# Kernel tuning notes

Measured on AMD Instinct MI355X. Metric: run time of the kernel, lower is better.

Reference implementation:

```python
import jax, jax.numpy as jnp
import numpy as np

B = 16384        # batch
P = 8            # num policies (experts)
D = 512          # latent dim
A = 64           # action dim
H = 1024         # hidden dim


def setup_inputs() -> dict:
    key = jax.random.key(0)
    ks = jax.random.split(key, 7)
    latents = jax.random.normal(ks[0], (B, D), dtype=jnp.float32)
    actions = jax.random.normal(ks[1], (B, A), dtype=jnp.float32)
    policy_indices = jax.random.randint(ks[2], (B,), 0, P, dtype=jnp.int64)
    # Per-policy 2-layer MLP params: concat(latent, action) -> hidden -> latent
    scale1 = 1.0 / np.sqrt(D + A)
    scale2 = 1.0 / np.sqrt(H)
    W1 = jax.random.normal(ks[3], (P, D + A, H), dtype=jnp.float32) * scale1
    b1 = jnp.zeros((P, H), dtype=jnp.float32)
    W2 = jax.random.normal(ks[4], (P, H, D), dtype=jnp.float32) * scale2
    b2 = jnp.zeros((P, D), dtype=jnp.float32)
    return {"latents": latents, "actions": actions, "policy_indices": policy_indices,
            "W1": W1, "b1": b1, "W2": W2, "b2": b2}


def reference(latents, actions, policy_indices, W1, b1, W2, b2):
    # Original: for each policy i, route rows with policy_indices == i through
    # that policy's dynamics model; scatter results back into next_latents.
    # Equivalent dense form: run all experts, then select per-row expert output.
    x = jnp.concatenate([latents, actions], axis=-1)          # [B, D+A]
    h = jax.nn.relu(jnp.einsum('bd,pdh->bph', x, W1) + b1)    # [B, P, H]
    y = jnp.einsum('bph,phd->bpd', h, W2) + b2                # [B, P, D]
    idx = policy_indices[:, None, None]                       # [B, 1, 1]
    next_latents = jnp.take_along_axis(y, idx, axis=1)[:, 0]  # [B, D]
    return next_latents
```

## Files before the change

### kernel.cpp

```cpp
#include <hip/hip_runtime.h>
#include <hip/hip_bf16.h>
#include <stdint.h>

#define B_SZ 16384
#define P_SZ 8
#define D_SZ 512
#define A_SZ 64
#define K1 576
#define H_SZ 1024
#define NSEG 64
#define MB_MAX 72
#define BPAD (B_SZ + P_SZ*256)
#define PREP_BLOCKS (BPAD * 72 / 256)
#define TR1_BLOCKS (P_SZ * 9 * 16)
#define TR2_BLOCKS (P_SZ * 16 * 8)
#define G1_GRID (BPAD / 128 * (H_SZ / 128))
#define G2_GRID (BPAD / 128 * (D_SZ / 64))

typedef __bf16 bf16_t;
typedef __bf16 bf16x8 __attribute__((ext_vector_type(8)));
typedef float f32x4 __attribute__((ext_vector_type(4)));

__device__ __forceinline__ void glds16(const void* g, void* l) {
    __builtin_amdgcn_global_load_lds(
        (const __attribute__((address_space(1))) unsigned*)g,
        (__attribute__((address_space(3))) unsigned*)l, 16, 0, 0);
}


__global__ __launch_bounds__(256) void hist_block(const int* __restrict__ pol,
                                                  int* __restrict__ blockhist,
                                                  int* __restrict__ rowidx) {
    __shared__ int lc[P_SZ];
    int t = threadIdx.x;
    if (t < P_SZ) lc[t] = 0;
    __syncthreads();
    int gid = blockIdx.x * 256 + t;
    rowidx[gid] = -1;
    if (gid < BPAD - B_SZ) rowidx[B_SZ + gid] = -1;
    atomicAdd(&lc[pol[gid]], 1);
    __syncthreads();
    if (t < P_SZ) blockhist[blockIdx.x * P_SZ + t] = lc[t];
}

__global__ __launch_bounds__(256) void prefix_kernel(const int* __restrict__ blockhist,
                                                     int* __restrict__ counts,
                                                     int* __restrict__ cursors,
                                                     int* __restrict__ blk_p) {
    __shared__ int csh[P_SZ];
    int t = threadIdx.x;
    int p = t >> 5, i = t & 31;
    int s = blockhist[i * P_SZ + p] + blockhist[(i + 32) * P_SZ + p];
#pragma unroll
    for (int m = 16; m >= 1; m >>= 1) s += __shfl_xor(s, m, 32);
    if (i == 0) csh[p] = s;
    __syncthreads();
    if (t == 0) {
        int run = 0;
        for (int pp = 0; pp < P_SZ; ++pp) {
            counts[pp] = csh[pp];
            cursors[pp] = run;
            run += ((csh[pp] + 255) >> 8) * 256;
        }
    }
    if (t < MB_MAX) {
        int run = 0, val = -1;
#pragma unroll
        for (int pp = 0; pp < P_SZ; ++pp) {
            int nb = (csh[pp] + 255) >> 8;
            if (t >= run && t < run + nb) val = pp;
            run += nb;
        }
        blk_p[t] = val;
    }
}

__global__ __launch_bounds__(256) void scatter_agg(const int* __restrict__ pol,
                                                   int* __restrict__ cursors,
                                                   int* __restrict__ rowidx) {
    __shared__ int lc[P_SZ], base_s[P_SZ];
    int t = threadIdx.x;
    if (t < P_SZ) lc[t] = 0;
    __syncthreads();
    int i = blockIdx.x * 256 + t;
    int p = pol[i];
    int lpos = atomicAdd(&lc[p], 1);
    __syncthreads();
    if (t < P_SZ) base_s[t] = atomicAdd(&cursors[t], lc[t]);
    __syncthreads();
    rowidx[base_s[p] + lpos] = i;
}


__global__ __launch_bounds__(256) void prep_all(const float* __restrict__ latents,
                                                const float* __restrict__ actions,
                                                const int* __restrict__ rowidx,
                                                const float* __restrict__ W1,
                                                const float* __restrict__ W2,
                                                bf16_t* __restrict__ xs,
                                                bf16_t* __restrict__ w1t,
                                                bf16_t* __restrict__ w2t) {
    int bx = blockIdx.x;
    int tid = threadIdx.x;
    if (bx < PREP_BLOCKS) {
        int idx = bx * 256 + tid;
        int s = idx / 72;
        int col = (idx - s * 72) * 8;
        int g = rowidx[s];
        bf16x8 o;
        if (g < 0) {
            o = (bf16x8){0,0,0,0,0,0,0,0};
        } else {
            const float* src;
            if (col < D_SZ) src = latents + (size_t)g * D_SZ + col;
            else            src = actions + (size_t)g * A_SZ + (col - D_SZ);
            f32x4 v0 = *(const f32x4*)src;
            f32x4 v1 = *(const f32x4*)(src + 4);
            o[0] = (bf16_t)v0[0]; o[1] = (bf16_t)v0[1]; o[2] = (bf16_t)v0[2]; o[3] = (bf16_t)v0[3];
            o[4] = (bf16_t)v1[0]; o[5] = (bf16_t)v1[1]; o[6] = (bf16_t)v1[2]; o[7] = (bf16_t)v1[3];
        }
        *(bf16x8*)(xs + (size_t)s * K1 + col) = o;
        return;
    }
    int tz = bx - PREP_BLOCKS;
    const float* Wp; bf16_t* WTp; int K, N, k0, n0;
    if (tz < TR1_BLOCKS) {
        int p = tz / 144, rem = tz % 144;
        k0 = (rem / 16) * 64; n0 = (rem % 16) * 64;
        K = K1; N = H_SZ;
        Wp = W1 + (size_t)p * K1 * H_SZ;
        WTp = w1t + (size_t)p * H_SZ * K1;
    } else {
        int u = tz - TR1_BLOCKS;
        int p = u / 128, rem = u % 128;
        k0 = (rem / 8) * 64; n0 = (rem % 8) * 64;
        K = H_SZ; N = D_SZ;
        Wp = W2 + (size_t)p * H_SZ * D_SZ;
        WTp = w2t + (size_t)p * D_SZ * H_SZ;
    }
    __shared__ float ls[64][65];
#pragma unroll
    for (int e = 0; e < 4; ++e) {
        int idx = e * 256 + tid;
        int kk = idx >> 4, nn = (idx & 15) * 4;
        f32x4 v = *(const f32x4*)&Wp[(size_t)(k0 + kk) * N + n0 + nn];
        ls[kk][nn]     = v[0];
        ls[kk][nn + 1] = v[1];
        ls[kk][nn + 2] = v[2];
        ls[kk][nn + 3] = v[3];
    }
    __syncthreads();
#pragma unroll
    for (int e = 0; e < 2; ++e) {
        int idx = e * 256 + tid;
        int nn = idx >> 3, ks = (idx & 7) * 8;
        bf16x8 o;
#pragma unroll
        for (int q = 0; q < 8; ++q) o[q] = (bf16_t)ls[ks + q][nn];
        *(bf16x8*)&WTp[(size_t)(n0 + nn) * K + k0 + ks] = o;
    }
}


__global__ __launch_bounds__(256, 3) void gemm1_kernel(
    const bf16_t* __restrict__ xs, const bf16_t* __restrict__ w1t,
    const float* __restrict__ b1, const int* __restrict__ blk_p,
    bf16_t* __restrict__ h) {

    const int b = blockIdx.x;
    const int wid = (b & 7) * (G1_GRID / 8) + (b >> 3);
    const int mb = wid >> 3;
    const int nb = wid & 7;
    const int p = blk_p[mb >> 1];
    if (p < 0) return;
    const int m0 = mb * 128;
    const int n0 = nb * 128;

    constexpr int SUB = 128 * 32;
    __shared__ __align__(16) bf16_t As[2 * SUB];
    __shared__ __align__(16) bf16_t Bs[2 * SUB];

    const int tid = threadIdx.x;
    const int wave = tid >> 6, lane = tid & 63;

    const bf16_t *a_src[2][2], *b_src[2][2];
    bf16_t *a_dst[2][2], *b_dst[2][2];
#pragma unroll
    for (int hh = 0; hh < 2; ++hh)
#pragma unroll
        for (int i = 0; i < 2; ++i) {
            int c = (wave * 2 + i) * 64 + lane;
            int r = c >> 2;
            int kl = (c & 3) ^ ((r >> 1) & 3);
            a_src[hh][i] = xs + (size_t)(m0 + r) * K1 + hh * 32 + kl * 8;
            a_dst[hh][i] = As + hh * SUB + c * 8;
            b_src[hh][i] = w1t + ((size_t)p * H_SZ + n0 + r) * K1 + hh * 32 + kl * 8;
            b_dst[hh][i] = Bs + hh * SUB + c * 8;
        }

    const int l16 = lane & 15, qd = lane >> 4;
    const int swz = (l16 >> 1) & 3;
    const int wr = wave >> 1, wc = wave & 1;
    int aoff[4], boff[4];
#pragma unroll
    for (int i = 0; i < 4; ++i) aoff[i] = (wr * 64 + i * 16 + l16) * 32 + ((qd ^ swz) * 8);
#pragma unroll
    for (int j = 0; j < 4; ++j) boff[j] = (wc * 64 + j * 16 + l16) * 32 + ((qd ^ swz) * 8);

    f32x4 acc[4][4];
#pragma unroll
    for (int i = 0; i < 4; ++i)
#pragma unroll
        for (int j = 0; j < 4; ++j)
            acc[i][j] = (f32x4){0.f, 0.f, 0.f, 0.f};

    for (int kt = 0; kt < K1; kt += 64) {
        __syncthreads();
#pragma unroll
        for (int hh = 0; hh < 2; ++hh)
#pragma unroll
            for (int i = 0; i < 2; ++i) {
                glds16(a_src[hh][i] + kt, a_dst[hh][i]);
                glds16(b_src[hh][i] + kt, b_dst[hh][i]);
            }
        __syncthreads();
#pragma unroll
        for (int hh = 0; hh < 2; ++hh) {
            bf16x8 af[4], bfv[4];
#pragma unroll
            for (int i = 0; i < 4; ++i) af[i] = *(const bf16x8*)(As + hh * SUB + aoff[i]);
#pragma unroll
            for (int j = 0; j < 4; ++j) bfv[j] = *(const bf16x8*)(Bs + hh * SUB + boff[j]);
#pragma unroll
            for (int i = 0; i < 4; ++i)
#pragma unroll
                for (int j = 0; j < 4; ++j)
                    acc[i][j] = __builtin_amdgcn_mfma_f32_16x16x32_bf16(af[i], bfv[j], acc[i][j], 0, 0, 0);
        }
    }

#pragma unroll
    for (int i = 0; i < 4; ++i) {
#pragma unroll
        for (int r = 0; r < 4; ++r) {
            int ml = wr * 64 + i * 16 + qd * 4 + r;
            size_t row = (size_t)(m0 + ml);
#pragma unroll
            for (int j = 0; j < 4; ++j) {
                int n = n0 + wc * 64 + j * 16 + l16;
                float v = acc[i][j][r] + b1[p * H_SZ + n];
                h[row * H_SZ + n] = (bf16_t)fmaxf(v, 0.f);
            }
        }
    }
}

__global__ __launch_bounds__(256, 4) void gemm2_kernel(
    const bf16_t* __restrict__ h, const bf16_t* __restrict__ w2t,
    const float* __restrict__ b2, const int* __restrict__ blk_p,
    const int* __restrict__ rowidx, float* __restrict__ out) {

    const int b = blockIdx.x;
    const int wid = (b & 7) * (G2_GRID / 8) + (b >> 3);
    const int mb = wid >> 3;
    const int nb = wid & 7;
    const int p = blk_p[mb >> 1];
    if (p < 0) return;
    const int m0 = mb * 128;
    const int n0 = nb * 64;

    constexpr int ASUB = 128 * 32;
    constexpr int BSUB = 64 * 32;
    __shared__ __align__(16) bf16_t As[2 * ASUB];
    __shared__ __align__(16) bf16_t Bs[2 * BSUB];

    const int tid = threadIdx.x;
    const int wave = tid >> 6, lane = tid & 63;

    const bf16_t *a_src[2][2]; bf16_t *a_dst[2][2];
#pragma unroll
    for (int hh = 0; hh < 2; ++hh)
#pragma unroll
        for (int i = 0; i < 2; ++i) {
            int c = (wave * 2 + i) * 64 + lane;
            int r = c >> 2;
            int kl = (c & 3) ^ ((r >> 1) & 3);
            a_src[hh][i] = h + (size_t)(m0 + r) * H_SZ + hh * 32 + kl * 8;
            a_dst[hh][i] = As + hh * ASUB + c * 8;
        }
    const bf16_t *b_src[2]; bf16_t *b_dst[2];
#pragma unroll
    for (int hh = 0; hh < 2; ++hh) {
        int c = wave * 64 + lane;
        int r = c >> 2;
        int kl = (c & 3) ^ ((r >> 1) & 3);
        b_src[hh] = w2t + ((size_t)p * D_SZ + n0 + r) * H_SZ + hh * 32 + kl * 8;
        b_dst[hh] = Bs + hh * BSUB + c * 8;
    }

    const int l16 = lane & 15, qd = lane >> 4;
    const int swz = (l16 >> 1) & 3;
    const int wr = wave >> 1, wc = wave & 1;
    int aoff[4], boff[2];
#pragma unroll
    for (int i = 0; i < 4; ++i) aoff[i] = (wr * 64 + i * 16 + l16) * 32 + ((qd ^ swz) * 8);
#pragma unroll
    for (int j = 0; j < 2; ++j) boff[j] = (wc * 32 + j * 16 + l16) * 32 + ((qd ^ swz) * 8);

    f32x4 acc[4][2];
#pragma unroll
    for (int i = 0; i < 4; ++i)
#pragma unroll
        for (int j = 0; j < 2; ++j)
            acc[i][j] = (f32x4){0.f, 0.f, 0.f, 0.f};

    for (int kt = 0; kt < H_SZ; kt += 64) {
        __syncthreads();
#pragma unroll
        for (int hh = 0; hh < 2; ++hh) {
#pragma unroll
            for (int i = 0; i < 2; ++i) glds16(a_src[hh][i] + kt, a_dst[hh][i]);
            glds16(b_src[hh] + kt, b_dst[hh]);
        }
        __syncthreads();
#pragma unroll
        for (int hh = 0; hh < 2; ++hh) {
            bf16x8 af[4], bfv[2];
#pragma unroll
            for (int i = 0; i < 4; ++i) af[i] = *(const bf16x8*)(As + hh * ASUB + aoff[i]);
#pragma unroll
            for (int j = 0; j < 2; ++j) bfv[j] = *(const bf16x8*)(Bs + hh * BSUB + boff[j]);
#pragma unroll
            for (int i = 0; i < 4; ++i)
#pragma unroll
                for (int j = 0; j < 2; ++j)
                    acc[i][j] = __builtin_amdgcn_mfma_f32_16x16x32_bf16(af[i], bfv[j], acc[i][j], 0, 0, 0);
        }
    }

#pragma unroll
    for (int i = 0; i < 4; ++i) {
#pragma unroll
        for (int r = 0; r < 4; ++r) {
            int ml = wr * 64 + i * 16 + qd * 4 + r;
            int g = rowidx[m0 + ml];
            if (g >= 0) {
                size_t orow = (size_t)g * D_SZ;
#pragma unroll
                for (int j = 0; j < 2; ++j) {
                    int n = n0 + wc * 32 + j * 16 + l16;
                    out[orow + n] = acc[i][j][r] + b2[p * D_SZ + n];
                }
            }
        }
    }
}


extern "C" void kernel_launch(void* const* d_in, const int* in_sizes, int n_in,
                              void* d_out, int out_size, void* d_ws, size_t ws_size,
                              hipStream_t stream) {
    const float* latents = (const float*)d_in[0];
    const float* actions = (const float*)d_in[1];
    const int*   pol     = (const int*)d_in[2];
    const float* W1      = (const float*)d_in[3];
    const float* b1      = (const float*)d_in[4];
    const float* W2      = (const float*)d_in[5];
    const float* b2      = (const float*)d_in[6];
    float* out = (float*)d_out;

    char* ws = (char*)d_ws;
    int* counts    = (int*)ws;
    int* cursors   = counts + P_SZ;
    int* blk_p     = cursors + P_SZ;
    int* blockhist = blk_p + MB_MAX;
    int* rowidx    = blockhist + NSEG * P_SZ;
    size_t pos = ((size_t)(2 * P_SZ + MB_MAX + NSEG * P_SZ + BPAD) * sizeof(int) + 255) & ~(size_t)255;
    bf16_t* xs  = (bf16_t*)(ws + pos);  pos += (size_t)BPAD * K1 * 2;
    bf16_t* hbuf= (bf16_t*)(ws + pos);  pos += (size_t)BPAD * H_SZ * 2;
    bf16_t* w1t = (bf16_t*)(ws + pos);  pos += (size_t)P_SZ * H_SZ * K1 * 2;
    bf16_t* w2t = (bf16_t*)(ws + pos);  pos += (size_t)P_SZ * D_SZ * H_SZ * 2;

    hist_block<<<NSEG, 256, 0, stream>>>(pol, blockhist, rowidx);
    prefix_kernel<<<1, 256, 0, stream>>>(blockhist, counts, cursors, blk_p);
    scatter_agg<<<NSEG, 256, 0, stream>>>(pol, cursors, rowidx);
    prep_all<<<PREP_BLOCKS + TR1_BLOCKS + TR2_BLOCKS, 256, 0, stream>>>(
        latents, actions, rowidx, W1, W2, xs, w1t, w2t);
    gemm1_kernel<<<G1_GRID, 256, 0, stream>>>(xs, w1t, b1, blk_p, hbuf);
    gemm2_kernel<<<G2_GRID, 256, 0, stream>>>(hbuf, w2t, b2, blk_p, rowidx, out);
}
```

Before: 192.6 us.

## Double-buffer LDS tiles in both GEMMs to overlap global loads with MFMA

Both grouped GEMM kernels now hold two LDS buffers per operand. Each iteration issues the async global-to-LDS loads for the next K-tile right after a single barrier, then runs MFMAs on the current tile, so memory latency overlaps with compute and one of the two barriers per iteration is gone. This doubles LDS use per block, so the launch-bounds occupancy hints drop from 3 to 2 (gemm1) and from 4 to 3 (gemm2). Fewer resident blocks per CU can hide less latency across warps.

```diff
diff --git a/kernel.cpp b/kernel.cpp
--- a/kernel.cpp
+++ b/kernel.cpp
@@ -162,7 +162,7 @@
 }
 
 
-__global__ __launch_bounds__(256, 3) void gemm1_kernel(
+__global__ __launch_bounds__(256, 2) void gemm1_kernel(
     const bf16_t* __restrict__ xs, const bf16_t* __restrict__ w1t,
     const float* __restrict__ b1, const int* __restrict__ blk_p,
     bf16_t* __restrict__ h) {
@@ -177,14 +177,15 @@
     const int n0 = nb * 128;
 
     constexpr int SUB = 128 * 32;
-    __shared__ __align__(16) bf16_t As[2 * SUB];
-    __shared__ __align__(16) bf16_t Bs[2 * SUB];
+    constexpr int BUF = 2 * SUB;
+    __shared__ __align__(16) bf16_t As[2 * BUF];
+    __shared__ __align__(16) bf16_t Bs[2 * BUF];
 
     const int tid = threadIdx.x;
     const int wave = tid >> 6, lane = tid & 63;
 
     const bf16_t *a_src[2][2], *b_src[2][2];
-    bf16_t *a_dst[2][2], *b_dst[2][2];
+    int a_slot[2][2], b_slot[2][2];
 #pragma unroll
     for (int hh = 0; hh < 2; ++hh)
 #pragma unroll
@@ -193,10 +194,23 @@
             int r = c >> 2;
             int kl = (c & 3) ^ ((r >> 1) & 3);
             a_src[hh][i] = xs + (size_t)(m0 + r) * K1 + hh * 32 + kl * 8;
-            a_dst[hh][i] = As + hh * SUB + c * 8;
             b_src[hh][i] = w1t + ((size_t)p * H_SZ + n0 + r) * K1 + hh * 32 + kl * 8;
-            b_dst[hh][i] = Bs + hh * SUB + c * 8;
-        }
+            a_slot[hh][i] = hh * SUB + c * 8;
+            b_slot[hh][i] = hh * SUB + c * 8;
+        }
+
+    auto stage = [&](int kt, int buf) {
+        const int bo = buf * BUF;
+#pragma unroll
+        for (int hh = 0; hh < 2; ++hh)
+#pragma unroll
+            for (int i = 0; i < 2; ++i) {
+                glds16(a_src[hh][i] + kt, As + bo + a_slot[hh][i]);
+                glds16(b_src[hh][i] + kt, Bs + bo + b_slot[hh][i]);
+            }
+    };
+
+    stage(0, 0);
 
     const int l16 = lane & 15, qd = lane >> 4;
     const int swz = (l16 >> 1) & 3;
@@ -214,23 +228,18 @@
         for (int j = 0; j < 4; ++j)
             acc[i][j] = (f32x4){0.f, 0.f, 0.f, 0.f};
 
-    for (int kt = 0; kt < K1; kt += 64) {
+    constexpr int NT = K1 / 64;
+    for (int t = 0; t < NT; ++t) {
         __syncthreads();
-#pragma unroll
-        for (int hh = 0; hh < 2; ++hh)
-#pragma unroll
-            for (int i = 0; i < 2; ++i) {
-                glds16(a_src[hh][i] + kt, a_dst[hh][i]);
-                glds16(b_src[hh][i] + kt, b_dst[hh][i]);
-            }
-        __syncthreads();
+        if (t + 1 < NT) stage((t + 1) * 64, (t + 1) & 1);
+        const int bo = (t & 1) * BUF;
 #pragma unroll
         for (int hh = 0; hh < 2; ++hh) {
             bf16x8 af[4], bfv[4];
 #pragma unroll
-            for (int i = 0; i < 4; ++i) af[i] = *(const bf16x8*)(As + hh * SUB + aoff[i]);
-#pragma unroll
-            for (int j = 0; j < 4; ++j) bfv[j] = *(const bf16x8*)(Bs + hh * SUB + boff[j]);
+            for (int i = 0; i < 4; ++i) af[i] = *(const bf16x8*)(As + bo + hh * SUB + aoff[i]);
+#pragma unroll
+            for (int j = 0; j < 4; ++j) bfv[j] = *(const bf16x8*)(Bs + bo + hh * SUB + boff[j]);
 #pragma unroll
             for (int i = 0; i < 4; ++i)
 #pragma unroll
@@ -255,7 +264,7 @@
     }
 }
 
-__global__ __launch_bounds__(256, 4) void gemm2_kernel(
+__global__ __launch_bounds__(256, 3) void gemm2_kernel(
     const bf16_t* __restrict__ h, const bf16_t* __restrict__ w2t,
     const float* __restrict__ b2, const int* __restrict__ blk_p,
     const int* __restrict__ rowidx, float* __restrict__ out) {
@@ -270,14 +279,16 @@
     const int n0 = nb * 64;
 
     constexpr int ASUB = 128 * 32;
+    constexpr int ABUF = 2 * ASUB;
     constexpr int BSUB = 64 * 32;
-    __shared__ __align__(16) bf16_t As[2 * ASUB];
-    __shared__ __align__(16) bf16_t Bs[2 * BSUB];
+    constexpr int BBUF = 2 * BSUB;
+    __shared__ __align__(16) bf16_t As[2 * ABUF];
+    __shared__ __align__(16) bf16_t Bs[2 * BBUF];
 
     const int tid = threadIdx.x;
     const int wave = tid >> 6, lane = tid & 63;
 
-    const bf16_t *a_src[2][2]; bf16_t *a_dst[2][2];
+    const bf16_t *a_src[2][2]; int a_slot[2][2];
 #pragma unroll
     for (int hh = 0; hh < 2; ++hh)
 #pragma unroll
@@ -286,17 +297,29 @@
             int r = c >> 2;
             int kl = (c & 3) ^ ((r >> 1) & 3);
             a_src[hh][i] = h + (size_t)(m0 + r) * H_SZ + hh * 32 + kl * 8;
-            a_dst[hh][i] = As + hh * ASUB + c * 8;
-        }
-    const bf16_t *b_src[2]; bf16_t *b_dst[2];
+            a_slot[hh][i] = hh * ASUB + c * 8;
+        }
+    const bf16_t *b_src[2]; int b_slot[2];
 #pragma unroll
     for (int hh = 0; hh < 2; ++hh) {
         int c = wave * 64 + lane;
         int r = c >> 2;
         int kl = (c & 3) ^ ((r >> 1) & 3);
         b_src[hh] = w2t + ((size_t)p * D_SZ + n0 + r) * H_SZ + hh * 32 + kl * 8;
-        b_dst[hh] = Bs + hh * BSUB + c * 8;
-    }
+        b_slot[hh] = hh * BSUB + c * 8;
+    }
+
+    auto stage = [&](int kt, int buf) {
+#pragma unroll
+        for (int hh = 0; hh < 2; ++hh) {
+#pragma unroll
+            for (int i = 0; i < 2; ++i)
+                glds16(a_src[hh][i] + kt, As + buf * ABUF + a_slot[hh][i]);
+            glds16(b_src[hh] + kt, Bs + buf * BBUF + b_slot[hh]);
+        }
+    };
+
+    stage(0, 0);
 
     const int l16 = lane & 15, qd = lane >> 4;
     const int swz = (l16 >> 1) & 3;
@@ -314,22 +337,19 @@
         for (int j = 0; j < 2; ++j)
             acc[i][j] = (f32x4){0.f, 0.f, 0.f, 0.f};
 
-    for (int kt = 0; kt < H_SZ; kt += 64) {
+    constexpr int NT = H_SZ / 64;
+    for (int t = 0; t < NT; ++t) {
         __syncthreads();
-#pragma unroll
-        for (int hh = 0; hh < 2; ++hh) {
-#pragma unroll
-            for (int i = 0; i < 2; ++i) glds16(a_src[hh][i] + kt, a_dst[hh][i]);
-            glds16(b_src[hh] + kt, b_dst[hh]);
-        }
-        __syncthreads();
+        if (t + 1 < NT) stage((t + 1) * 64, (t + 1) & 1);
+        const int ao = (t & 1) * ABUF;
+        const int bo = (t & 1) * BBUF;
 #pragma unroll
         for (int hh = 0; hh < 2; ++hh) {
             bf16x8 af[4], bfv[2];
 #pragma unroll
-            for (int i = 0; i < 4; ++i) af[i] = *(const bf16x8*)(As + hh * ASUB + aoff[i]);
-#pragma unroll
-            for (int j = 0; j < 2; ++j) bfv[j] = *(const bf16x8*)(Bs + hh * BSUB + boff[j]);
+            for (int i = 0; i < 4; ++i) af[i] = *(const bf16x8*)(As + ao + hh * ASUB + aoff[i]);
+#pragma unroll
+            for (int j = 0; j < 2; ++j) bfv[j] = *(const bf16x8*)(Bs + bo + hh * BSUB + boff[j]);
 #pragma unroll
             for (int i = 0; i < 4; ++i)
 #pragma unroll
```

Result: slower. 215.1 us (+11.7%).

## Drop LDS staging in expert GEMMs and load MFMA fragments directly from global

Applied to the files above, without the earlier changes.

Both grouped GEMM kernels stop staging tiles through shared memory with global_load_lds and barriers. Each wave now reads its A and B fragments directly from global memory (via cache) into registers for a private 64x64 output tile. The block tile changes to 64 rows by 256 columns, and gemm2 goes from 128x64 to 64x256 with a 4x4 accumulator per wave. This removes LDS traffic and __syncthreads, but gives up reuse of tiles across waves, so it relies on L1/L2 hits. It also adds uncoalesced 16-byte strided global loads with no prefetch or overlap.

```diff
diff --git a/kernel.cpp b/kernel.cpp
--- a/kernel.cpp
+++ b/kernel.cpp
@@ -14,18 +14,12 @@
 #define PREP_BLOCKS (BPAD * 72 / 256)
 #define TR1_BLOCKS (P_SZ * 9 * 16)
 #define TR2_BLOCKS (P_SZ * 16 * 8)
-#define G1_GRID (BPAD / 128 * (H_SZ / 128))
-#define G2_GRID (BPAD / 128 * (D_SZ / 64))
+#define G1_GRID (BPAD / 64 * (H_SZ / 64) / 4)
+#define G2_GRID (BPAD / 64 * (D_SZ / 64) / 4)
 
 typedef __bf16 bf16_t;
 typedef __bf16 bf16x8 __attribute__((ext_vector_type(8)));
 typedef float f32x4 __attribute__((ext_vector_type(4)));
-
-__device__ __forceinline__ void glds16(const void* g, void* l) {
-    __builtin_amdgcn_global_load_lds(
-        (const __attribute__((address_space(1))) unsigned*)g,
-        (__attribute__((address_space(3))) unsigned*)l, 16, 0, 0);
-}
 
 
 __global__ __launch_bounds__(256) void hist_block(const int* __restrict__ pol,
@@ -162,50 +156,33 @@
 }
 
 
-__global__ __launch_bounds__(256, 3) void gemm1_kernel(
+__global__ __launch_bounds__(256, 2) void gemm1_kernel(
     const bf16_t* __restrict__ xs, const bf16_t* __restrict__ w1t,
     const float* __restrict__ b1, const int* __restrict__ blk_p,
     bf16_t* __restrict__ h) {
 
     const int b = blockIdx.x;
     const int wid = (b & 7) * (G1_GRID / 8) + (b >> 3);
-    const int mb = wid >> 3;
-    const int nb = wid & 7;
-    const int p = blk_p[mb >> 1];
+    const int mb = wid >> 2;
+    const int nblk = wid & 3;
+    const int p = blk_p[mb >> 2];
     if (p < 0) return;
-    const int m0 = mb * 128;
-    const int n0 = nb * 128;
-
-    constexpr int SUB = 128 * 32;
-    __shared__ __align__(16) bf16_t As[2 * SUB];
-    __shared__ __align__(16) bf16_t Bs[2 * SUB];
 
     const int tid = threadIdx.x;
     const int wave = tid >> 6, lane = tid & 63;
-
-    const bf16_t *a_src[2][2], *b_src[2][2];
-    bf16_t *a_dst[2][2], *b_dst[2][2];
-#pragma unroll
-    for (int hh = 0; hh < 2; ++hh)
-#pragma unroll
-        for (int i = 0; i < 2; ++i) {
-            int c = (wave * 2 + i) * 64 + lane;
-            int r = c >> 2;
-            int kl = (c & 3) ^ ((r >> 1) & 3);
-            a_src[hh][i] = xs + (size_t)(m0 + r) * K1 + hh * 32 + kl * 8;
-            a_dst[hh][i] = As + hh * SUB + c * 8;
-            b_src[hh][i] = w1t + ((size_t)p * H_SZ + n0 + r) * K1 + hh * 32 + kl * 8;
-            b_dst[hh][i] = Bs + hh * SUB + c * 8;
-        }
-
     const int l16 = lane & 15, qd = lane >> 4;
-    const int swz = (l16 >> 1) & 3;
-    const int wr = wave >> 1, wc = wave & 1;
-    int aoff[4], boff[4];
-#pragma unroll
-    for (int i = 0; i < 4; ++i) aoff[i] = (wr * 64 + i * 16 + l16) * 32 + ((qd ^ swz) * 8);
-#pragma unroll
-    for (int j = 0; j < 4; ++j) boff[j] = (wc * 64 + j * 16 + l16) * 32 + ((qd ^ swz) * 8);
+
+    const int m0 = mb * 64;
+    const int n0 = (nblk * 4 + wave) * 64;
+
+    const bf16_t* arow[4];
+    const bf16_t* brow[4];
+#pragma unroll
+    for (int i = 0; i < 4; ++i)
+        arow[i] = xs + (size_t)(m0 + i * 16 + l16) * K1 + qd * 8;
+#pragma unroll
+    for (int j = 0; j < 4; ++j)
+        brow[j] = w1t + ((size_t)p * H_SZ + n0 + j * 16 + l16) * K1 + qd * 8;
 
     f32x4 acc[4][4];
 #pragma unroll
@@ -214,40 +191,28 @@
         for (int j = 0; j < 4; ++j)
             acc[i][j] = (f32x4){0.f, 0.f, 0.f, 0.f};
 
-    for (int kt = 0; kt < K1; kt += 64) {
-        __syncthreads();
-#pragma unroll
-        for (int hh = 0; hh < 2; ++hh)
-#pragma unroll
-            for (int i = 0; i < 2; ++i) {
-                glds16(a_src[hh][i] + kt, a_dst[hh][i]);
-                glds16(b_src[hh][i] + kt, b_dst[hh][i]);
-            }
-        __syncthreads();
-#pragma unroll
-        for (int hh = 0; hh < 2; ++hh) {
-            bf16x8 af[4], bfv[4];
-#pragma unroll
-            for (int i = 0; i < 4; ++i) af[i] = *(const bf16x8*)(As + hh * SUB + aoff[i]);
-#pragma unroll
-            for (int j = 0; j < 4; ++j) bfv[j] = *(const bf16x8*)(Bs + hh * SUB + boff[j]);
-#pragma unroll
-            for (int i = 0; i < 4; ++i)
-#pragma unroll
-                for (int j = 0; j < 4; ++j)
-                    acc[i][j] = __builtin_amdgcn_mfma_f32_16x16x32_bf16(af[i], bfv[j], acc[i][j], 0, 0, 0);
-        }
+    for (int kt = 0; kt < K1; kt += 32) {
+        bf16x8 af[4], bfv[4];
+#pragma unroll
+        for (int i = 0; i < 4; ++i) af[i] = *(const bf16x8*)(arow[i] + kt);
+#pragma unroll
+        for (int j = 0; j < 4; ++j) bfv[j] = *(const bf16x8*)(brow[j] + kt);
+#pragma unroll
+        for (int i = 0; i < 4; ++i)
+#pragma unroll
+            for (int j = 0; j < 4; ++j)
+                acc[i][j] = __builtin_amdgcn_mfma_f32_16x16x32_bf16(af[i], bfv[j], acc[i][j], 0, 0, 0);
     }
 
 #pragma unroll
     for (int i = 0; i < 4; ++i) {
 #pragma unroll
         for (int r = 0; r < 4; ++r) {
-            int ml = wr * 64 + i * 16 + qd * 4 + r;
+            int ml = i * 16 + qd * 4 + r;
             size_t row = (size_t)(m0 + ml);
 #pragma unroll
             for (int j = 0; j < 4; ++j) {
-                int n = n0 + wc * 64 + j * 16 + l16;
+                int n = n0 + j * 16 + l16;
                 float v = acc[i][j][r] + b1[p * H_SZ + n];
                 h[row * H_SZ + n] = (bf16_t)fmaxf(v, 0.f);
             }
@@ -255,100 +220,65 @@
     }
 }
 
-__global__ __launch_bounds__(256, 4) void gemm2_kernel(
+__global__ __launch_bounds__(256, 2) void gemm2_kernel(
     const bf16_t* __restrict__ h, const bf16_t* __restrict__ w2t,
     const float* __restrict__ b2, const int* __restrict__ blk_p,
     const int* __restrict__ rowidx, float* __restrict__ out) {
 
     const int b = blockIdx.x;
     const int wid = (b & 7) * (G2_GRID / 8) + (b >> 3);
-    const int mb = wid >> 3;
-    const int nb = wid & 7;
-    const int p = blk_p[mb >> 1];
+    const int mb = wid >> 1;
+    const int nblk = wid & 1;
+    const int p = blk_p[mb >> 2];
     if (p < 0) return;
-    const int m0 = mb * 128;
-    const int n0 = nb * 64;
-
-    constexpr int ASUB = 128 * 32;
-    constexpr int BSUB = 64 * 32;
-    __shared__ __align__(16) bf16_t As[2 * ASUB];
-    __shared__ __align__(16) bf16_t Bs[2 * BSUB];
 
     const int tid = threadIdx.x;
     const int wave = tid >> 6, lane = tid & 63;
-
-    const bf16_t *a_src[2][2]; bf16_t *a_dst[2][2];
-#pragma unroll
-    for (int hh = 0; hh < 2; ++hh)
-#pragma unroll
-        for (int i = 0; i < 2; ++i) {
-            int c = (wave * 2 + i) * 64 + lane;
-            int r = c >> 2;
-            int kl = (c & 3) ^ ((r >> 1) & 3);
-            a_src[hh][i] = h + (size_t)(m0 + r) * H_SZ + hh * 32 + kl * 8;
-            a_dst[hh][i] = As + hh * ASUB + c * 8;
-        }
-    const bf16_t *b_src[2]; bf16_t *b_dst[2];
-#pragma unroll
-    for (int hh = 0; hh < 2; ++hh) {
-        int c = wave * 64 + lane;
-        int r = c >> 2;
-        int kl = (c & 3) ^ ((r >> 1) & 3);
-        b_src[hh] = w2t + ((size_t)p * D_SZ + n0 + r) * H_SZ + hh * 32 + kl * 8;
-        b_dst[hh] = Bs + hh * BSUB + c * 8;
-    }
-
     const int l16 = lane & 15, qd = lane >> 4;
-    const int swz = (l16 >> 1) & 3;
-    const int wr = wave >> 1, wc = wave & 1;
-    int aoff[4], boff[2];
-#pragma unroll
-    for (int i = 0; i < 4; ++i) aoff[i] = (wr * 64 + i * 16 + l16) * 32 + ((qd ^ swz) * 8);
-#pragma unroll
-    for (int j = 0; j < 2; ++j) boff[j] = (wc * 32 + j * 16 + l16) * 32 + ((qd ^ swz) * 8);
-
-    f32x4 acc[4][2];
+
+    const int m0 = mb * 64;
+    const int n0 = (nblk * 4 + wave) * 64;
+
+    const bf16_t* arow[4];
+    const bf16_t* brow[4];
 #pragma unroll
     for (int i = 0; i < 4; ++i)
-#pragma unroll
-        for (int j = 0; j < 2; ++j)
+        arow[i] = h + (size_t)(m0 + i * 16 + l16) * H_SZ + qd * 8;
+#pragma unroll
+    for (int j = 0; j < 4; ++j)
+        brow[j] = w2t + ((size_t)p * D_SZ + n0 + j * 16 + l16) * H_SZ + qd * 8;
+
+    f32x4 acc[4][4];
+#pragma unroll
+    for (int i = 0; i < 4; ++i)
+#pragma unroll
+        for (int j = 0; j < 4; ++j)
             acc[i][j] = (f32x4){0.f, 0.f, 0.f, 0.f};
 
-    for (int kt = 0; kt < H_SZ; kt += 64) {
-        __syncthreads();
-#pragma unroll
-        for (int hh = 0; hh < 2; ++hh) {
-#pragma unroll
-            for (int i = 0; i < 2; ++i) glds16(a_src[hh][i] + kt, a_dst[hh][i]);
-            glds16(b_src[hh] + kt, b_dst[hh]);
-        }
-        __syncthreads();
-#pragma unroll
-        for (int hh = 0; hh < 2; ++hh) {
-            bf16x8 af[4], bfv[2];
-#pragma unroll
-            for (int i = 0; i < 4; ++i) af[i] = *(const bf16x8*)(As + hh * ASUB + aoff[i]);
-#pragma unroll
-            for (int j = 0; j < 2; ++j) bfv[j] = *(const bf16x8*)(Bs + hh * BSUB + boff[j]);
-#pragma unroll
-            for (int i = 0; i < 4; ++i)
-#pragma unroll
-                for (int j = 0; j < 2; ++j)
-                    acc[i][j] = __builtin_amdgcn_mfma_f32_16x16x32_bf16(af[i], bfv[j], acc[i][j], 0, 0, 0);
-        }
+    for (int kt = 0; kt < H_SZ; kt += 32) {
+        bf16x8 af[4], bfv[4];
+#pragma unroll
+        for (int i = 0; i < 4; ++i) af[i] = *(const bf16x8*)(arow[i] + kt);
+#pragma unroll
+        for (int j = 0; j < 4; ++j) bfv[j] = *(const bf16x8*)(brow[j] + kt);
+#pragma unroll
+        for (int i = 0; i < 4; ++i)
+#pragma unroll
+            for (int j = 0; j < 4; ++j)
+                acc[i][j] = __builtin_amdgcn_mfma_f32_16x16x32_bf16(af[i], bfv[j], acc[i][j], 0, 0, 0);
     }
 
 #pragma unroll
     for (int i = 0; i < 4; ++i) {
 #pragma unroll
         for (int r = 0; r < 4; ++r) {
-            int ml = wr * 64 + i * 16 + qd * 4 + r;
+            int ml = i * 16 + qd * 4 + r;
             int g = rowidx[m0 + ml];
             if (g >= 0) {
                 size_t orow = (size_t)g * D_SZ;
 #pragma unroll
-                for (int j = 0; j < 2; ++j) {
-                    int n = n0 + wc * 32 + j * 16 + l16;
+                for (int j = 0; j < 4; ++j) {
+                    int n = n0 + j * 16 + l16;
                     out[orow + n] = acc[i][j][r] + b2[p * D_SZ + n];
                 }
             }
```

Result: slower. 310.1 us (+61.0%).
